# Kernel optimization log

Hardware: AMD Instinct MI355X
Metric: run time of the kernel (lower is better)

## Reference

```python
import jax, jax.numpy as jnp
import numpy as np

VOXEL_SIZE = 0.04


def setup_inputs() -> dict:
    key = jax.random.key(0)
    k1, k2, k3 = jax.random.split(key, 3)
    N, V, C, H, W = 262144, 9, 24, 120, 160
    NVOX = 64
    # sparse voxel coords (N,4): [batch_ind=0, x, y, z]
    xyz = jax.random.randint(k1, (N, 3), 0, NVOX + 1, dtype=jnp.int32)
    coords = jnp.concatenate([jnp.zeros((N, 1), jnp.int32), xyz], axis=1)
    # volume origin chosen so world z is in front of the cameras
    origin = jnp.array([[-1.28, -1.28, 0.5]], dtype=jnp.float32)
    feats = jax.random.normal(k2, (V, C, H, W), dtype=jnp.float32)
    # realistic pinhole projections K @ [I | t_v] (4x4)
    fx = fy = 80.0
    cx, cy = (W - 1) / 2.0, (H - 1) / 2.0
    K = jnp.array([[fx, 0.0, cx], [0.0, fy, cy], [0.0, 0.0, 1.0]], jnp.float32)
    t = jax.random.uniform(k3, (V, 3), minval=-0.1, maxval=0.1, dtype=jnp.float32)
    Rt = jnp.concatenate([jnp.broadcast_to(jnp.eye(3, dtype=jnp.float32), (V, 3, 3)), t[:, :, None]], axis=2)  # (V,3,4)
    P3 = jnp.einsum('ij,vjk->vik', K, Rt)  # (V,3,4)
    last = jnp.broadcast_to(jnp.array([[0.0, 0.0, 0.0, 1.0]], jnp.float32), (V, 1, 4))
    proj = jnp.concatenate([P3, last], axis=1)  # (V,4,4)
    return {"coords": coords, "origin": origin, "feats": feats, "proj": proj}


def _back_project(coords, origin, feats, proj):
    V, C, H, W = feats.shape
    # voxel grid -> world coords
    world = coords[:, 1:].astype(jnp.float32) * VOXEL_SIZE + origin[0]  # (N,3)
    wh = jnp.concatenate([world, jnp.ones_like(world[:, :1])], axis=1)  # (N,4)
    # project into every view
    im_p = jnp.einsum('vij,nj->vni', proj, wh)  # (V,N,4)
    im_x, im_y, im_z = im_p[..., 0], im_p[..., 1], im_p[..., 2]
    px = im_x / im_z  # pixel coords (align_corners=True grid maps back to pixels)
    py = im_y / im_z
    in_bounds = (px >= 0) & (px <= W - 1) & (py >= 0) & (py <= H - 1) & (im_z > 0)  # (V,N)

    # bilinear gather with zero padding
    feats_vhwc = jnp.transpose(feats, (0, 2, 3, 1))  # (V,H,W,C)
    x0 = jnp.floor(px)
    y0 = jnp.floor(py)
    wx1 = px - x0
    wy1 = py - y0
    x0i = x0.astype(jnp.int32)
    y0i = y0.astype(jnp.int32)
    vidx = jnp.arange(V, dtype=jnp.int32)[:, None]

    def corner(xi, yi, w):
        valid = (xi >= 0) & (xi < W) & (yi >= 0) & (yi < H)
        xc = jnp.clip(xi, 0, W - 1)
        yc = jnp.clip(yi, 0, H - 1)
        f = feats_vhwc[vidx, yc, xc]  # (V,N,C) irregular gather
        return f * (w * valid)[..., None]

    samp = (corner(x0i, y0i, (1 - wx1) * (1 - wy1))
            + corner(x0i + 1, y0i, wx1 * (1 - wy1))
            + corner(x0i, y0i + 1, (1 - wx1) * wy1)
            + corner(x0i + 1, y0i + 1, wx1 * wy1))  # (V,N,C)

    samp = samp * in_bounds[..., None]
    z = im_z * in_bounds

    count = jnp.sum(in_bounds.astype(jnp.float32), axis=0)  # (N,)
    valid = count > 0
    denom = jnp.where(valid, count, 1.0)
    vol_feat = jnp.sum(samp, axis=0) / denom[:, None]  # (N,C)

    # normalized mean depth channel
    zsum = jnp.sum(z, axis=0) / denom  # (N,)
    n_valid = jnp.maximum(jnp.sum(valid.astype(jnp.float32)), 1.0)
    zmean = jnp.sum(zsum * valid) / n_valid
    diff = (zsum - zmean) * valid
    zstd = jnp.sqrt(jnp.sum(diff * diff)) + 1e-5  # torch.norm of masked vector
    znorm = jnp.where(valid, (zsum - zmean) / zstd, 0.0)

    volume = jnp.concatenate([vol_feat, znorm[:, None]], axis=1)  # (N,C+1)
    return volume, count


def reference(coords, origin, feats, proj):
    return _back_project(coords, origin, feats, proj)
```

## Files before the change

### kernel.cpp

```cpp
#include <hip/hip_runtime.h>
#include <hip/hip_fp16.h>
#include <math.h>

#define VOXSZ 0.04f
#define NV 9
#define NC 24
#define NH 120
#define NW 160
#define NBINS 262144
#define TBLOCKS (NV * NH)
#define PLANE_BYTES ((size_t)NV * NH * NW * 16)


__device__ __forceinline__ int morton6(int a) {
  a = (a | (a << 8)) & 0x300F;
  a = (a | (a << 4)) & 0x30C3;
  a = (a | (a << 2)) & 0x9249;
  return a;
}

__device__ __forceinline__ int voxel_key(int4 cd) {
  int x = min(max(cd.y, 0), 63), y = min(max(cd.z, 0), 63), z = min(max(cd.w, 0), 63);
  return morton6(x) | (morton6(y) << 1) | (morton6(z) << 2);
}

__global__ __launch_bounds__(256)
void zero_hist_k(int4* __restrict__ hist4) {
  hist4[blockIdx.x * 256 + threadIdx.x] = make_int4(0, 0, 0, 0);
}

__global__ __launch_bounds__(256)
void prep_k(const float* __restrict__ feats, __half* __restrict__ outT,
            const int4* __restrict__ coords, const float* __restrict__ origin,
            const float* __restrict__ proj, int* __restrict__ hist,
            double* __restrict__ partials, float* __restrict__ out, int N) {
  __shared__ __half s[NC][NW + 2];
  __shared__ float s_proj[NV * 12];
  __shared__ float s_org[3];
  __shared__ double s_red[3][4];
  int tid = threadIdx.x;

  if (blockIdx.x < TBLOCKS) {
    int vh = blockIdx.x;
    int v = vh / NH, h = vh % NH;
    const float* ibase = feats + (size_t)v * NC * NH * NW + (size_t)h * NW;
    for (int e = tid; e < NC * (NW / 4); e += 256) {
      int c = e / (NW / 4), w4 = e - c * (NW / 4);
      float4 f = *(const float4*)(ibase + (size_t)c * NH * NW + w4 * 4);
      int w = w4 * 4;
      s[c][w]     = __float2half(f.x);
      s[c][w + 1] = __float2half(f.y);
      s[c][w + 2] = __float2half(f.z);
      s[c][w + 3] = __float2half(f.w);
    }
    __syncthreads();
    for (int j = tid; j < NW * 12; j += 256) {
      int p = j / (NW * 4);
      int rem = j - p * (NW * 4);
      int w = rem >> 2, k = rem & 3;
      __half2 hv = __halves2half2(s[8 * p + 2 * k][w], s[8 * p + 2 * k + 1][w]);
      unsigned int* obase =
          (unsigned int*)((char*)outT + (size_t)p * PLANE_BYTES) + (size_t)vh * NW * 4;
      obase[(w << 2) | k] = *(unsigned int*)&hv;
    }
    return;
  }

  if (tid < NV * 12) s_proj[tid] = proj[(tid / 12) * 16 + (tid % 12)];
  if (tid < 3) s_org[tid] = origin[tid];
  __syncthreads();

  int sid = blockIdx.x - TBLOCKS;
  int n = sid * 256 + tid;
  double rz = 0.0, rz2 = 0.0, rv = 0.0;
  if (n < N) {
    int4 cd = coords[n];
    atomicAdd(&hist[voxel_key(cd)], 1);
    float wx = (float)cd.y * VOXSZ + s_org[0];
    float wy = (float)cd.z * VOXSZ + s_org[1];
    float wz = (float)cd.w * VOXSZ + s_org[2];
    float zs = 0.f; int cnt = 0;
#pragma unroll
    for (int v = 0; v < NV; ++v) {
      const float* P = &s_proj[v * 12];
      float ix = P[0] * wx + P[1] * wy + P[2]  * wz + P[3];
      float iy = P[4] * wx + P[5] * wy + P[6]  * wz + P[7];
      float iz = P[8] * wx + P[9] * wy + P[10] * wz + P[11];
      float px = ix / iz, py = iy / iz;
      bool inb = (px >= 0.f) && (px <= (float)(NW - 1)) &&
                 (py >= 0.f) && (py <= (float)(NH - 1)) && (iz > 0.f);
      if (inb) { cnt++; zs += iz; }
    }
    out[(size_t)N * (NC + 1) + n] = (float)cnt;
    if (cnt > 0) {
      float zsv = zs / (float)cnt;
      rz = (double)zsv; rz2 = (double)zsv * (double)zsv; rv = 1.0;
    }
  }
#pragma unroll
  for (int off = 32; off > 0; off >>= 1) {
    rz  += __shfl_down(rz,  off, 64);
    rz2 += __shfl_down(rz2, off, 64);
    rv  += __shfl_down(rv,  off, 64);
  }
  if ((tid & 63) == 0) {
    int w = tid >> 6;
    s_red[0][w] = rz; s_red[1][w] = rz2; s_red[2][w] = rv;
  }
  __syncthreads();
  if (tid == 0) {
    double a = 0, b = 0, c = 0;
#pragma unroll
    for (int w = 0; w < 4; ++w) { a += s_red[0][w]; b += s_red[1][w]; c += s_red[2][w]; }
    double* p = partials + (size_t)sid * 4;
    p[0] = a; p[1] = b; p[2] = c;
  }
}

__global__ __launch_bounds__(256)
void scanA_k(const int* __restrict__ hist, int* __restrict__ bsum,
             const double* __restrict__ partials, int nblocks,
             float* __restrict__ scal) {
  int tid = threadIdx.x;

  if (blockIdx.x == 256) {
    double rz = 0.0, rz2 = 0.0, rv = 0.0;
    for (int i = tid; i < nblocks; i += 256) {
      const double* p = partials + (size_t)i * 4;
      rz += p[0]; rz2 += p[1]; rv += p[2];
    }
#pragma unroll
    for (int off = 32; off > 0; off >>= 1) {
      rz  += __shfl_down(rz,  off, 64);
      rz2 += __shfl_down(rz2, off, 64);
      rv  += __shfl_down(rv,  off, 64);
    }
    __shared__ double s[3][4];
    if ((tid & 63) == 0) {
      int w = tid >> 6;
      s[0][w] = rz; s[1][w] = rz2; s[2][w] = rv;
    }
    __syncthreads();
    if (tid == 0) {
      double sz = 0, sz2 = 0, nv = 0;
#pragma unroll
      for (int w = 0; w < 4; ++w) { sz += s[0][w]; sz2 += s[1][w]; nv += s[2][w]; }
      double nvm = (nv > 1.0) ? nv : 1.0;
      double zmean = sz / nvm;
      double var = sz2 - 2.0 * zmean * sz + zmean * zmean * nv;
      if (var < 0.0) var = 0.0;
      double zstd = sqrt(var) + 1e-5;
      scal[0] = (float)zmean;
      scal[1] = (float)zstd;
    }
    return;
  }

  __shared__ int red[256];
  const int4* h4 = (const int4*)hist;
  int4 h = h4[blockIdx.x * 256 + tid];
  red[tid] = h.x + h.y + h.z + h.w;
  __syncthreads();
  for (int off = 128; off > 0; off >>= 1) {
    if (tid < off) red[tid] += red[tid + off];
    __syncthreads();
  }
  if (tid == 0) bsum[blockIdx.x] = red[0];
}

__global__ __launch_bounds__(256)
void scanB_k(const int* __restrict__ hist, const int* __restrict__ bsum,
             int* __restrict__ ofs) {
  __shared__ int sb[256];
  __shared__ int st[256];
  int tid = threadIdx.x;

  sb[tid] = bsum[tid];
  __syncthreads();
  for (int off = 1; off < 256; off <<= 1) {
    int v = (tid >= off) ? sb[tid - off] : 0;
    __syncthreads();
    sb[tid] += v;
    __syncthreads();
  }
  int base_blk = (blockIdx.x == 0) ? 0 : sb[blockIdx.x - 1];

  const int4* h4 = (const int4*)hist;
  int4* o4 = (int4*)ofs;
  int idx = blockIdx.x * 256 + tid;
  int4 h = h4[idx];
  int tsum = h.x + h.y + h.z + h.w;
  st[tid] = tsum;
  __syncthreads();
  for (int off = 1; off < 256; off <<= 1) {
    int v = (tid >= off) ? st[tid - off] : 0;
    __syncthreads();
    st[tid] += v;
    __syncthreads();
  }
  int base = base_blk + st[tid] - tsum;
  int4 o;
  o.x = base;
  o.y = base + h.x;
  o.z = o.y + h.y;
  o.w = o.z + h.z;
  o4[idx] = o;
}

__global__ __launch_bounds__(256)
void scatter_k(const int4* __restrict__ coords, int* __restrict__ ofs,
               int2* __restrict__ sorted, int N) {
  int n = blockIdx.x * blockDim.x + threadIdx.x;
  if (n >= N) return;
  int4 cd = coords[n];
  int pos = atomicAdd(&ofs[voxel_key(cd)], 1);
  sorted[pos] = make_int2(cd.y | (cd.z << 7) | (cd.w << 14), n);
}

__global__ __launch_bounds__(192, 4)
void bp_gather_k(const int2* __restrict__ sorted, const float* __restrict__ origin,
                 const float* __restrict__ proj, const __half* __restrict__ featsT,
                 const float* __restrict__ scal, float* __restrict__ out, int N) {
  __shared__ float s_proj[NV * 12];
  __shared__ float s_org[3];
  __shared__ float s_scal[2];
  __shared__ uint2 s_offd[NV][64];
  __shared__ uint4 s_w2[NV][64];
  __shared__ float s_zs[3][64];
  __shared__ int   s_cnt[3][64];
  int tid = threadIdx.x;
  if (tid < NV * 12) s_proj[tid] = proj[(tid / 12) * 16 + (tid % 12)];
  if (tid < 3) s_org[tid] = origin[tid];
  if (tid < 2) s_scal[tid] = scal[tid];
  __syncthreads();

  int nwg = gridDim.x, orig = blockIdx.x;
  int xcd = orig & 7, q = nwg >> 3, r = nwg & 7;
  int bid = (xcd < r ? xcd * (q + 1) : r * (q + 1) + (xcd - r) * q) + (orig >> 3);

  int lane = tid & 63, part = tid >> 6;
  int i = bid * 64 + lane;
  int n = -1, xi = 0, yi = 0, zi = 0;
  if (i < N) {
    int2 rec = sorted[i];
    n = rec.y;
    xi = rec.x & 127; yi = (rec.x >> 7) & 127; zi = (rec.x >> 14) & 127;
  }
  float wx = (float)xi * VOXSZ + s_org[0];
  float wy = (float)yi * VOXSZ + s_org[1];
  float wz = (float)zi * VOXSZ + s_org[2];
  float vm = (n >= 0) ? 1.f : 0.f;

  float zsp = 0.f; int cntp = 0;
#pragma unroll
  for (int qv = 0; qv < 3; ++qv) {
    int v = 3 * part + qv;
    const float* P = &s_proj[v * 12];
    float ix = P[0] * wx + P[1] * wy + P[2]  * wz + P[3];
    float iy = P[4] * wx + P[5] * wy + P[6]  * wz + P[7];
    float iz = P[8] * wx + P[9] * wy + P[10] * wz + P[11];
    float px = ix / iz, py = iy / iz;
    bool inb = (px >= 0.f) && (px <= (float)(NW - 1)) &&
               (py >= 0.f) && (py <= (float)(NH - 1)) && (iz > 0.f);
    float wm = inb ? vm : 0.f;
    cntp += (wm > 0.f) ? 1 : 0;
    zsp = fmaf(wm, iz, zsp);
    float pxc = fminf(fmaxf(px, 0.f), (float)(NW - 1));
    float pyc = fminf(fmaxf(py, 0.f), (float)(NH - 1));
    float x0f = floorf(pxc), y0f = floorf(pyc);
    float fx1 = pxc - x0f, fy1 = pyc - y0f;
    float fx0 = 1.f - fx1, fy0 = 1.f - fy1;
    int x0 = (int)x0f, y0 = (int)y0f;
    unsigned dx = (x0 + 1 < NW) ? 16u : 0u;
    unsigned dy = (y0 + 1 < NH) ? (unsigned)(NW * 16) : 0u;
    unsigned off = (unsigned)(((y0 + v * NH) * NW + x0) * 16);
    __half2 h00 = __float2half2_rn(fx0 * fy0 * wm);
    __half2 h10 = __float2half2_rn(fx1 * fy0 * wm);
    __half2 h01 = __float2half2_rn(fx0 * fy1 * wm);
    __half2 h11 = __float2half2_rn(fx1 * fy1 * wm);
    s_offd[v][lane] = make_uint2(off, dx | (dy << 16));
    uint4 wv;
    wv.x = *(unsigned int*)&h00;
    wv.y = *(unsigned int*)&h10;
    wv.z = *(unsigned int*)&h01;
    wv.w = *(unsigned int*)&h11;
    s_w2[v][lane] = wv;
  }
  s_zs[part][lane] = zsp;
  s_cnt[part][lane] = cntp;
  __syncthreads();

  int cnt = s_cnt[0][lane] + s_cnt[1][lane] + s_cnt[2][lane];
  __half2 acc2[4];
  const __half2 zero2 = __float2half2_rn(0.f);
#pragma unroll
  for (int c = 0; c < 4; ++c) acc2[c] = zero2;
  const char* fbase = (const char*)featsT + (size_t)part * PLANE_BYTES;

#pragma unroll
  for (int v = 0; v < NV; ++v) {
    uint4 wv = s_w2[v][lane];
    if ((wv.x | wv.y | wv.z | wv.w) == 0u) continue;
    uint2 od = s_offd[v][lane];
    unsigned dx = od.y & 0xFFFFu, dy = od.y >> 16;
    const char* p00 = fbase + od.x;
    float4 c00 = *(const float4*)p00;
    float4 c10 = *(const float4*)(p00 + dx);
    float4 c01 = *(const float4*)(p00 + dy);
    float4 c11 = *(const float4*)(p00 + dx + dy);
    __half2 w00 = *(__half2*)&wv.x;
    __half2 w10 = *(__half2*)&wv.y;
    __half2 w01 = *(__half2*)&wv.z;
    __half2 w11 = *(__half2*)&wv.w;
    const __half2* h00 = (const __half2*)&c00;
    const __half2* h10 = (const __half2*)&c10;
    const __half2* h01 = (const __half2*)&c01;
    const __half2* h11 = (const __half2*)&c11;
#pragma unroll
    for (int c = 0; c < 4; ++c) acc2[c] = __hfma2(w00, h00[c], acc2[c]);
#pragma unroll
    for (int c = 0; c < 4; ++c) acc2[c] = __hfma2(w10, h10[c], acc2[c]);
#pragma unroll
    for (int c = 0; c < 4; ++c) acc2[c] = __hfma2(w01, h01[c], acc2[c]);
#pragma unroll
    for (int c = 0; c < 4; ++c) acc2[c] = __hfma2(w11, h11[c], acc2[c]);
  }

  if (n < 0) return;
  float denom = (cnt > 0) ? (float)cnt : 1.f;
  float inv = 1.f / denom;
  size_t row = (size_t)n * (NC + 1) + part * 8;
#pragma unroll
  for (int c = 0; c < 4; ++c) {
    float2 t = __half22float2(acc2[c]);
    out[row + 2 * c]     = t.x * inv;
    out[row + 2 * c + 1] = t.y * inv;
  }
  if (part == 2) {
    float zs = s_zs[0][lane] + s_zs[1][lane] + s_zs[2][lane];
    float zsv = zs * inv;
    out[(size_t)n * (NC + 1) + NC] = (cnt > 0) ? (zsv - s_scal[0]) / s_scal[1] : 0.f;
  }
}

__global__ __launch_bounds__(256)
void stats_k(const int4* __restrict__ coords, const float* __restrict__ origin,
             const float* __restrict__ proj, double* __restrict__ partials, int N) {
  __shared__ float s_proj[NV * 12];
  __shared__ float s_org[3];
  __shared__ double s_red[3][4];
  int tid = threadIdx.x;
  if (tid < NV * 12) s_proj[tid] = proj[(tid / 12) * 16 + (tid % 12)];
  if (tid < 3) s_org[tid] = origin[tid];
  __syncthreads();
  int n = blockIdx.x * blockDim.x + tid;
  double rz = 0.0, rz2 = 0.0, rv = 0.0;
  if (n < N) {
    int4 cd = coords[n];
    float wx = (float)cd.y * VOXSZ + s_org[0];
    float wy = (float)cd.z * VOXSZ + s_org[1];
    float wz = (float)cd.w * VOXSZ + s_org[2];
    float zs = 0.f; int cnt = 0;
#pragma unroll
    for (int v = 0; v < NV; ++v) {
      const float* P = &s_proj[v * 12];
      float ix = P[0] * wx + P[1] * wy + P[2]  * wz + P[3];
      float iy = P[4] * wx + P[5] * wy + P[6]  * wz + P[7];
      float iz = P[8] * wx + P[9] * wy + P[10] * wz + P[11];
      float px = ix / iz, py = iy / iz;
      bool inb = (px >= 0.f) && (px <= (float)(NW - 1)) &&
                 (py >= 0.f) && (py <= (float)(NH - 1)) && (iz > 0.f);
      if (inb) { cnt++; zs += iz; }
    }
    if (cnt > 0) {
      float zsv = zs / (float)cnt;
      rz = (double)zsv; rz2 = (double)zsv * (double)zsv; rv = 1.0;
    }
  }
#pragma unroll
  for (int off = 32; off > 0; off >>= 1) {
    rz  += __shfl_down(rz,  off, 64);
    rz2 += __shfl_down(rz2, off, 64);
    rv  += __shfl_down(rv,  off, 64);
  }
  if ((tid & 63) == 0) {
    int w = tid >> 6;
    s_red[0][w] = rz; s_red[1][w] = rz2; s_red[2][w] = rv;
  }
  __syncthreads();
  if (tid == 0) {
    double a = 0, b = 0, c = 0;
#pragma unroll
    for (int w = 0; w < 4; ++w) { a += s_red[0][w]; b += s_red[1][w]; c += s_red[2][w]; }
    double* p = partials + (size_t)blockIdx.x * 4;
    p[0] = a; p[1] = b; p[2] = c;
  }
}

__global__ __launch_bounds__(1024)
void reduce_finalize_k(const double* __restrict__ partials, int nblocks,
                       float* __restrict__ scal) {
  int tid = threadIdx.x;
  double rz = 0.0, rz2 = 0.0, rv = 0.0;
  for (int i = tid; i < nblocks; i += 1024) {
    const double* p = partials + (size_t)i * 4;
    rz += p[0]; rz2 += p[1]; rv += p[2];
  }
#pragma unroll
  for (int off = 32; off > 0; off >>= 1) {
    rz  += __shfl_down(rz,  off, 64);
    rz2 += __shfl_down(rz2, off, 64);
    rv  += __shfl_down(rv,  off, 64);
  }
  __shared__ double s[3][16];
  if ((tid & 63) == 0) {
    int w = tid >> 6;
    s[0][w] = rz; s[1][w] = rz2; s[2][w] = rv;
  }
  __syncthreads();
  if (tid == 0) {
    double sz = 0, sz2 = 0, nv = 0;
#pragma unroll
    for (int w = 0; w < 16; ++w) { sz += s[0][w]; sz2 += s[1][w]; nv += s[2][w]; }
    double nvm = (nv > 1.0) ? nv : 1.0;
    double zmean = sz / nvm;
    double var = sz2 - 2.0 * zmean * sz + zmean * zmean * nv;
    if (var < 0.0) var = 0.0;
    double zstd = sqrt(var) + 1e-5;
    scal[0] = (float)zmean;
    scal[1] = (float)zstd;
  }
}

__global__ __launch_bounds__(256)
void bp_fallback_k(const int4* __restrict__ coords, const float* __restrict__ origin,
                   const float* __restrict__ proj, const float* __restrict__ feats,
                   const float* __restrict__ scal, float* __restrict__ out, int N) {
  __shared__ float s_proj[NV * 12];
  __shared__ float s_org[3];
  __shared__ float s_scal[2];
  int tid = threadIdx.x;
  if (tid < NV * 12) s_proj[tid] = proj[(tid / 12) * 16 + (tid % 12)];
  if (tid < 3) s_org[tid] = origin[tid];
  if (tid < 2) s_scal[tid] = scal[tid];
  __syncthreads();
  int n = blockIdx.x * blockDim.x + tid;
  if (n >= N) return;
  int4 cd = coords[n];
  float wx = (float)cd.y * VOXSZ + s_org[0];
  float wy = (float)cd.z * VOXSZ + s_org[1];
  float wz = (float)cd.w * VOXSZ + s_org[2];
  float acc[NC];
#pragma unroll
  for (int c = 0; c < NC; ++c) acc[c] = 0.f;
  float zs = 0.f; int cnt = 0;
#pragma unroll
  for (int v = 0; v < NV; ++v) {
    const float* P = &s_proj[v * 12];
    float ix = P[0] * wx + P[1] * wy + P[2]  * wz + P[3];
    float iy = P[4] * wx + P[5] * wy + P[6]  * wz + P[7];
    float iz = P[8] * wx + P[9] * wy + P[10] * wz + P[11];
    float px = ix / iz, py = iy / iz;
    bool inb = (px >= 0.f) && (px <= (float)(NW - 1)) &&
               (py >= 0.f) && (py <= (float)(NH - 1)) && (iz > 0.f);
    if (!inb) continue;
    cnt++; zs += iz;
    float x0f = floorf(px), y0f = floorf(py);
    float fx1 = px - x0f, fy1 = py - y0f;
    float fx0 = 1.f - fx1, fy0 = 1.f - fy1;
    int x0 = (int)x0f, y0 = (int)y0f;
    int x1 = (x0 + 1 < NW) ? x0 + 1 : NW - 1;
    int y1 = (y0 + 1 < NH) ? y0 + 1 : NH - 1;
    float w00 = fx0 * fy0, w10 = fx1 * fy0, w01 = fx0 * fy1, w11 = fx1 * fy1;
    const float* base = feats + (size_t)v * NC * NH * NW;
#pragma unroll
    for (int c = 0; c < NC; ++c) {
      const float* pc = base + (size_t)c * NH * NW;
      acc[c] += pc[y0 * NW + x0] * w00 + pc[y0 * NW + x1] * w10 +
                pc[y1 * NW + x0] * w01 + pc[y1 * NW + x1] * w11;
    }
  }
  float denom = (cnt > 0) ? (float)cnt : 1.f;
  float inv = 1.f / denom;
  size_t row = (size_t)n * (NC + 1);
#pragma unroll
  for (int c = 0; c < NC; ++c) out[row + c] = acc[c] * inv;
  float zsv = zs * inv;
  out[row + NC] = (cnt > 0) ? (zsv - s_scal[0]) / s_scal[1] : 0.f;
  out[(size_t)N * (NC + 1) + n] = (float)cnt;
}

extern "C" void kernel_launch(void* const* d_in, const int* in_sizes, int n_in,
                              void* d_out, int out_size, void* d_ws, size_t ws_size,
                              hipStream_t stream) {
  const int4*  coords = (const int4*)d_in[0];
  const float* origin = (const float*)d_in[1];
  const float* feats  = (const float*)d_in[2];
  const float* proj   = (const float*)d_in[3];
  float* out = (float*)d_out;
  int N = in_sizes[0] / 4;

  int blocksAll = (N + 255) / 256;

  char* ws = (char*)d_ws;
  float*  scal     = (float*)ws;
  double* partials = (double*)(ws + 64);
  size_t off = 64 + (size_t)blocksAll * 4 * sizeof(double);
  off = (off + 63) & ~(size_t)63;
  __half* featsT = (__half*)(ws + off);
  off += 3 * PLANE_BYTES;
  int* hist = (int*)(ws + off); off += (size_t)NBINS * sizeof(int);
  int* ofs  = (int*)(ws + off); off += (size_t)NBINS * sizeof(int);
  int* bsum = (int*)(ws + off); off += 256 * sizeof(int);
  off = (off + 15) & ~(size_t)15;
  int2* sorted = (int2*)(ws + off); off += (size_t)N * sizeof(int2);
  bool full = (ws_size >= off);

  if (full) {
    zero_hist_k<<<NBINS / 1024, 256, 0, stream>>>((int4*)hist);
    prep_k<<<TBLOCKS + blocksAll, 256, 0, stream>>>(feats, featsT, coords, origin,
                                                    proj, hist, partials, out, N);
    scanA_k<<<257, 256, 0, stream>>>(hist, bsum, partials, blocksAll, scal);
    scanB_k<<<256, 256, 0, stream>>>(hist, bsum, ofs);
    scatter_k<<<blocksAll, 256, 0, stream>>>(coords, ofs, sorted, N);
    int gblocks = (N + 63) / 64;
    bp_gather_k<<<gblocks, 192, 0, stream>>>(sorted, origin, proj, featsT, scal, out, N);
  } else {
    stats_k<<<blocksAll, 256, 0, stream>>>(coords, origin, proj, partials, N);
    reduce_finalize_k<<<1, 1024, 0, stream>>>(partials, blocksAll, scal);
    bp_fallback_k<<<blocksAll, 256, 0, stream>>>(coords, origin, proj, feats, scal, out, N);
  }
}
```

Measured before the change: 83.11 us.

## Fuse histogram, prep, scan and scatter into one cooperative persistent kernel

Merges the five pre-gather kernels (histogram zeroing, feature transpose/stats, block sums, prefix scan, scatter) into a single cooperative kernel of 512 persistent blocks that separates phases with grid.sync. The aim is to remove the per-launch gaps and tail effects between small kernels. In exchange it adds grid-wide barrier costs, serialises work onto a fixed grid (the 256 scan blocks and the scatter loop run on fewer resident blocks), and falls back to the old multi-kernel path if the cooperative launch fails.

```diff
diff --git a/kernel.cpp b/kernel.cpp
--- a/kernel.cpp
+++ b/kernel.cpp
@@ -1,6 +1,9 @@
 #include <hip/hip_runtime.h>
+#include <hip/hip_cooperative_groups.h>
 #include <hip/hip_fp16.h>
 #include <math.h>
+
+namespace cg = cooperative_groups;
 
 #define VOXSZ 0.04f
 #define NV 9
@@ -22,6 +25,195 @@
 __device__ __forceinline__ int voxel_key(int4 cd) {
   int x = min(max(cd.y, 0), 63), y = min(max(cd.z, 0), 63), z = min(max(cd.w, 0), 63);
   return morton6(x) | (morton6(y) << 1) | (morton6(z) << 2);
+}
+
+__global__ __launch_bounds__(256, 4)
+void fused_prep_sort_k(const float* __restrict__ feats, __half* __restrict__ featsT,
+                       const int4* __restrict__ coords, const float* __restrict__ origin,
+                       const float* __restrict__ proj, int* __restrict__ hist,
+                       int* __restrict__ ofs, int* __restrict__ bsum,
+                       double* __restrict__ partials, float* __restrict__ scal,
+                       int2* __restrict__ sorted, float* __restrict__ out, int N) {
+  cg::grid_group grid = cg::this_grid();
+  int tid = threadIdx.x;
+  int bid = blockIdx.x;
+  int G = gridDim.x;
+
+  __shared__ __half s[NC][NW + 2];
+  __shared__ float s_proj[NV * 12];
+  __shared__ float s_org[3];
+  __shared__ double s_red[3][4];
+  __shared__ int red[256];
+  __shared__ int sb[256];
+  __shared__ int st[256];
+
+  if (tid < NV * 12) s_proj[tid] = proj[(tid / 12) * 16 + (tid % 12)];
+  if (tid < 3) s_org[tid] = origin[tid];
+
+  const int SUNITS = (N + 255) / 256;
+
+  for (int i = bid * 256 + tid; i < NBINS / 4; i += G * 256)
+    ((int4*)hist)[i] = make_int4(0, 0, 0, 0);
+  grid.sync();
+
+  for (int u = bid; u < TBLOCKS + SUNITS; u += G) {
+    if (u < TBLOCKS) {
+      int v = u / NH, h = u % NH;
+      const float* ibase = feats + (size_t)v * NC * NH * NW + (size_t)h * NW;
+      for (int e = tid; e < NC * (NW / 4); e += 256) {
+        int c = e / (NW / 4), w4 = e - c * (NW / 4);
+        float4 f = *(const float4*)(ibase + (size_t)c * NH * NW + w4 * 4);
+        int w = w4 * 4;
+        s[c][w]     = __float2half(f.x);
+        s[c][w + 1] = __float2half(f.y);
+        s[c][w + 2] = __float2half(f.z);
+        s[c][w + 3] = __float2half(f.w);
+      }
+      __syncthreads();
+      for (int j = tid; j < NW * 12; j += 256) {
+        int p = j / (NW * 4);
+        int rem = j - p * (NW * 4);
+        int w = rem >> 2, k = rem & 3;
+        __half2 hv = __halves2half2(s[8 * p + 2 * k][w], s[8 * p + 2 * k + 1][w]);
+        unsigned int* obase =
+            (unsigned int*)((char*)featsT + (size_t)p * PLANE_BYTES) + (size_t)u * NW * 4;
+        obase[(w << 2) | k] = *(unsigned int*)&hv;
+      }
+      __syncthreads();
+    } else {
+      int sid = u - TBLOCKS;
+      int n = sid * 256 + tid;
+      double rz = 0.0, rz2 = 0.0, rv = 0.0;
+      if (n < N) {
+        int4 cd = coords[n];
+        atomicAdd(&hist[voxel_key(cd)], 1);
+        float wx = (float)cd.y * VOXSZ + s_org[0];
+        float wy = (float)cd.z * VOXSZ + s_org[1];
+        float wz = (float)cd.w * VOXSZ + s_org[2];
+        float zs = 0.f; int cnt = 0;
+#pragma unroll
+        for (int v = 0; v < NV; ++v) {
+          const float* P = &s_proj[v * 12];
+          float ix = P[0] * wx + P[1] * wy + P[2]  * wz + P[3];
+          float iy = P[4] * wx + P[5] * wy + P[6]  * wz + P[7];
+          float iz = P[8] * wx + P[9] * wy + P[10] * wz + P[11];
+          float px = ix / iz, py = iy / iz;
+          bool inb = (px >= 0.f) && (px <= (float)(NW - 1)) &&
+                     (py >= 0.f) && (py <= (float)(NH - 1)) && (iz > 0.f);
+          if (inb) { cnt++; zs += iz; }
+        }
+        out[(size_t)N * (NC + 1) + n] = (float)cnt;
+        if (cnt > 0) {
+          float zsv = zs / (float)cnt;
+          rz = (double)zsv; rz2 = (double)zsv * (double)zsv; rv = 1.0;
+        }
+      }
+#pragma unroll
+      for (int off = 32; off > 0; off >>= 1) {
+        rz  += __shfl_down(rz,  off, 64);
+        rz2 += __shfl_down(rz2, off, 64);
+        rv  += __shfl_down(rv,  off, 64);
+      }
+      if ((tid & 63) == 0) {
+        int w = tid >> 6;
+        s_red[0][w] = rz; s_red[1][w] = rz2; s_red[2][w] = rv;
+      }
+      __syncthreads();
+      if (tid == 0) {
+        double a = 0, b = 0, c = 0;
+#pragma unroll
+        for (int w = 0; w < 4; ++w) { a += s_red[0][w]; b += s_red[1][w]; c += s_red[2][w]; }
+        double* p = partials + (size_t)sid * 4;
+        p[0] = a; p[1] = b; p[2] = c;
+      }
+      __syncthreads();
+    }
+  }
+  grid.sync();
+
+  for (int u = bid; u < 257; u += G) {
+    if (u < 256) {
+      int4 h = ((const int4*)hist)[u * 256 + tid];
+      red[tid] = h.x + h.y + h.z + h.w;
+      __syncthreads();
+      for (int off = 128; off > 0; off >>= 1) {
+        if (tid < off) red[tid] += red[tid + off];
+        __syncthreads();
+      }
+      if (tid == 0) bsum[u] = red[0];
+      __syncthreads();
+    } else {
+      double rz = 0.0, rz2 = 0.0, rv = 0.0;
+      for (int i = tid; i < SUNITS; i += 256) {
+        const double* p = partials + (size_t)i * 4;
+        rz += p[0]; rz2 += p[1]; rv += p[2];
+      }
+#pragma unroll
+      for (int off = 32; off > 0; off >>= 1) {
+        rz  += __shfl_down(rz,  off, 64);
+        rz2 += __shfl_down(rz2, off, 64);
+        rv  += __shfl_down(rv,  off, 64);
+      }
+      if ((tid & 63) == 0) {
+        int w = tid >> 6;
+        s_red[0][w] = rz; s_red[1][w] = rz2; s_red[2][w] = rv;
+      }
+      __syncthreads();
+      if (tid == 0) {
+        double sz = 0, sz2 = 0, nv = 0;
+#pragma unroll
+        for (int w = 0; w < 4; ++w) { sz += s_red[0][w]; sz2 += s_red[1][w]; nv += s_red[2][w]; }
+        double nvm = (nv > 1.0) ? nv : 1.0;
+        double zmean = sz / nvm;
+        double var = sz2 - 2.0 * zmean * sz + zmean * zmean * nv;
+        if (var < 0.0) var = 0.0;
+        scal[0] = (float)zmean;
+        scal[1] = (float)(sqrt(var) + 1e-5);
+      }
+      __syncthreads();
+    }
+  }
+  grid.sync();
+
+  if (bid < 256) {
+    sb[tid] = bsum[tid];
+    __syncthreads();
+    for (int off = 1; off < 256; off <<= 1) {
+      int v = (tid >= off) ? sb[tid - off] : 0;
+      __syncthreads();
+      sb[tid] += v;
+      __syncthreads();
+    }
+    int base_blk = (bid == 0) ? 0 : sb[bid - 1];
+    int idx = bid * 256 + tid;
+    int4 h = ((const int4*)hist)[idx];
+    int tsum = h.x + h.y + h.z + h.w;
+    st[tid] = tsum;
+    __syncthreads();
+    for (int off = 1; off < 256; off <<= 1) {
+      int v = (tid >= off) ? st[tid - off] : 0;
+      __syncthreads();
+      st[tid] += v;
+      __syncthreads();
+    }
+    int base = base_blk + st[tid] - tsum;
+    int4 o;
+    o.x = base;
+    o.y = base + h.x;
+    o.z = o.y + h.y;
+    o.w = o.z + h.z;
+    ((int4*)ofs)[idx] = o;
+  }
+  grid.sync();
+
+  for (int u = bid; u < SUNITS; u += G) {
+    int n = u * 256 + tid;
+    if (n < N) {
+      int4 cd = coords[n];
+      int pos = atomicAdd(&ofs[voxel_key(cd)], 1);
+      sorted[pos] = make_int2(cd.y | (cd.z << 7) | (cd.w << 14), n);
+    }
+  }
 }
 
 __global__ __launch_bounds__(256)
@@ -122,7 +314,6 @@
              const double* __restrict__ partials, int nblocks,
              float* __restrict__ scal) {
   int tid = threadIdx.x;
-
   if (blockIdx.x == 256) {
     double rz = 0.0, rz2 = 0.0, rv = 0.0;
     for (int i = tid; i < nblocks; i += 256) {
@@ -149,16 +340,13 @@
       double zmean = sz / nvm;
       double var = sz2 - 2.0 * zmean * sz + zmean * zmean * nv;
       if (var < 0.0) var = 0.0;
-      double zstd = sqrt(var) + 1e-5;
       scal[0] = (float)zmean;
-      scal[1] = (float)zstd;
+      scal[1] = (float)(sqrt(var) + 1e-5);
     }
     return;
   }
-
   __shared__ int red[256];
-  const int4* h4 = (const int4*)hist;
-  int4 h = h4[blockIdx.x * 256 + tid];
+  int4 h = ((const int4*)hist)[blockIdx.x * 256 + tid];
   red[tid] = h.x + h.y + h.z + h.w;
   __syncthreads();
   for (int off = 128; off > 0; off >>= 1) {
@@ -174,7 +362,6 @@
   __shared__ int sb[256];
   __shared__ int st[256];
   int tid = threadIdx.x;
-
   sb[tid] = bsum[tid];
   __syncthreads();
   for (int off = 1; off < 256; off <<= 1) {
@@ -184,11 +371,8 @@
     __syncthreads();
   }
   int base_blk = (blockIdx.x == 0) ? 0 : sb[blockIdx.x - 1];
-
-  const int4* h4 = (const int4*)hist;
-  int4* o4 = (int4*)ofs;
   int idx = blockIdx.x * 256 + tid;
-  int4 h = h4[idx];
+  int4 h = ((const int4*)hist)[idx];
   int tsum = h.x + h.y + h.z + h.w;
   st[tid] = tsum;
   __syncthreads();
@@ -204,7 +388,7 @@
   o.y = base + h.x;
   o.z = o.y + h.y;
   o.w = o.z + h.z;
-  o4[idx] = o;
+  ((int4*)ofs)[idx] = o;
 }
 
 __global__ __launch_bounds__(256)
@@ -426,9 +610,8 @@
     double zmean = sz / nvm;
     double var = sz2 - 2.0 * zmean * sz + zmean * zmean * nv;
     if (var < 0.0) var = 0.0;
-    double zstd = sqrt(var) + 1e-5;
     scal[0] = (float)zmean;
-    scal[1] = (float)zstd;
+    scal[1] = (float)(sqrt(var) + 1e-5);
   }
 }
 
@@ -517,12 +700,20 @@
   bool full = (ws_size >= off);
 
   if (full) {
-    zero_hist_k<<<NBINS / 1024, 256, 0, stream>>>((int4*)hist);
-    prep_k<<<TBLOCKS + blocksAll, 256, 0, stream>>>(feats, featsT, coords, origin,
-                                                    proj, hist, partials, out, N);
-    scanA_k<<<257, 256, 0, stream>>>(hist, bsum, partials, blocksAll, scal);
-    scanB_k<<<256, 256, 0, stream>>>(hist, bsum, ofs);
-    scatter_k<<<blocksAll, 256, 0, stream>>>(coords, ofs, sorted, N);
+    void* kargs[] = {(void*)&feats, (void*)&featsT, (void*)&coords, (void*)&origin,
+                     (void*)&proj, (void*)&hist, (void*)&ofs, (void*)&bsum,
+                     (void*)&partials, (void*)&scal, (void*)&sorted, (void*)&out,
+                     (void*)&N};
+    hipError_t err = hipLaunchCooperativeKernel((const void*)fused_prep_sort_k,
+                                                dim3(512), dim3(256), kargs, 0, stream);
+    if (err != hipSuccess) {
+      zero_hist_k<<<NBINS / 1024, 256, 0, stream>>>((int4*)hist);
+      prep_k<<<TBLOCKS + blocksAll, 256, 0, stream>>>(feats, featsT, coords, origin,
+                                                      proj, hist, partials, out, N);
+      scanA_k<<<257, 256, 0, stream>>>(hist, bsum, partials, blocksAll, scal);
+      scanB_k<<<256, 256, 0, stream>>>(hist, bsum, ofs);
+      scatter_k<<<blocksAll, 256, 0, stream>>>(coords, ofs, sorted, N);
+    }
     int gblocks = (N + 63) / 64;
     bp_gather_k<<<gblocks, 192, 0, stream>>>(sorted, origin, proj, featsT, scal, out, N);
   } else {
```

New measurement: 284.3 us. +242.1%, slower.
